# Performance work log

Measured on AMD Instinct MI355X. Metric: run time of the kernel, lower is better.

The kernel has to match this reference:

```python
import jax, jax.numpy as jnp
import numpy as np

B, D, C = 4096, 256, 32000
T = 1.0
P_MARGIN = 0.5
N_MARGIN = 0.5
W_BU = 1.0
W_MS = 0.0
SIM_CAP = 0.999999


def setup_inputs() -> dict:
    key = jax.random.key(0)
    k1, k2, k3, k4, k5 = jax.random.split(key, 5)
    inputs = jax.random.normal(k1, (B, D), dtype=jnp.float32)
    inputs = inputs / jnp.linalg.norm(inputs, axis=1, keepdims=True)  # re-id features are L2-normalized
    targets = jax.random.randint(k2, (B,), 0, C, dtype=jnp.int32)
    indexs = jnp.arange(B, dtype=jnp.int32)
    label_to_pairs = jax.random.randint(k3, (B, 2), 0, B, dtype=jnp.int32)
    all_label_to_clusterid = jax.random.randint(k4, (C,), 0, C, dtype=jnp.int32)
    V = jax.random.normal(k5, (C, D), dtype=jnp.float32)
    V = V / jnp.linalg.norm(V, axis=1, keepdims=True)  # memory bank rows kept unit-norm by EMA update
    return {"inputs": inputs, "targets": targets, "indexs": indexs,
            "label_to_pairs": label_to_pairs,
            "all_label_to_clusterid": all_label_to_clusterid, "V": V}


def _ms_loss(inputs, targets):
    # vectorized form of ExLoss.ms with ms_table=False:
    # psims[i] = sims[i, targets==targets[i]], nsims[i] = sims[i, targets!=targets[i]]
    sims = inputs @ inputs.T  # [B, B]
    pos = targets[:, None] == targets[None, :]
    neg = ~pos
    NEG_BIG = jnp.float32(-1e30)
    POS_BIG = jnp.float32(1e30)
    p_thrd = jnp.where(neg.any(axis=1),
                       jnp.where(neg, sims, NEG_BIG).max(axis=1),
                       jnp.float32(-3.0)) + P_MARGIN
    n_thrd = jnp.where(pos.any(axis=1),
                       jnp.where(pos, sims, POS_BIG).min(axis=1),
                       jnp.float32(3.0)) - N_MARGIN
    hp = pos & (sims < p_thrd[:, None])
    hn = neg & (sims > n_thrd[:, None]) & (sims < SIM_CAP)
    hp_cnt = hp.sum()
    hn_cnt = hn.sum()
    # BCE-with-logits: target 1 -> softplus(-x); target 0 -> softplus(x); mean over kept elems
    hp_loss = jnp.where(hp_cnt > 0,
                        jnp.where(hp, jax.nn.softplus(-sims), 0.0).sum()
                        / jnp.maximum(hp_cnt, 1).astype(sims.dtype),
                        jnp.float32(0.0))
    hn_loss = jnp.where(hn_cnt > 0,
                        jnp.where(hn, jax.nn.softplus(sims), 0.0).sum()
                        / jnp.maximum(hn_cnt, 1).astype(sims.dtype),
                        jnp.float32(0.0))
    return hp_loss + hn_loss


def reference(inputs, targets, indexs, label_to_pairs, all_label_to_clusterid, V):
    # Exclusive.forward: logits against the memory bank
    tsims = inputs @ V.T            # [B, C]
    outputs = tsims * T
    # bu cross-entropy (weight=None, mean reduction)
    logp = jax.nn.log_softmax(outputs, axis=-1)
    bu_loss = -jnp.take_along_axis(logp, targets[:, None].astype(jnp.int32), axis=1).mean()
    ms_loss = _ms_loss(inputs, targets)
    loss = W_MS * ms_loss + W_BU * bu_loss
    return (loss, outputs)
```

## Files before the change

### kernel.cpp

```cpp
#include <hip/hip_runtime.h>
#include <hip/hip_bf16.h>
#include <stdint.h>

#define NB 4096
#define ND 256
#define NC 32000

typedef __bf16 bf16x8 __attribute__((ext_vector_type(8)));
typedef float  f32x4  __attribute__((ext_vector_type(4)));

#define GLDS16(g, l)                                                          \
  __builtin_amdgcn_global_load_lds(                                           \
      (const __attribute__((address_space(1))) void*)(g),                     \
      (__attribute__((address_space(3))) void*)(l), 16, 0, 0)

__device__ __forceinline__ unsigned short f32_to_bf16(float f) {
  union { float f; uint32_t u; } v; v.f = f;
  uint32_t r = v.u + 0x7fffu + ((v.u >> 16) & 1u);
  return (unsigned short)(r >> 16);
}

__global__ void prep_kernel(const float* __restrict__ inA,
                            const float* __restrict__ inV,
                            unsigned short* __restrict__ outA,
                            unsigned short* __restrict__ outV,
                            float* __restrict__ rowsum,
                            float* __restrict__ loss) {
  int gid = blockIdx.x * blockDim.x + threadIdx.x;
  int stride = gridDim.x * blockDim.x;
  if (gid == 0) *loss = 0.f;
  for (int i = gid; i < NB; i += stride) rowsum[i] = 0.f;
  const int nA4 = NB * ND / 4;
  const int nV4 = NC * ND / 4;
  for (int i = gid; i < nA4 + nV4; i += stride) {
    float4 v = (i < nA4) ? ((const float4*)inA)[i]
                         : ((const float4*)inV)[i - nA4];
    ushort4 o;
    o.x = f32_to_bf16(v.x);
    o.y = f32_to_bf16(v.y);
    o.z = f32_to_bf16(v.z);
    o.w = f32_to_bf16(v.w);
    if (i < nA4) ((ushort4*)outA)[i] = o;
    else         ((ushort4*)outV)[i - nA4] = o;
  }
}

__global__ void __launch_bounds__(256)
gemm_expsum_kernel(const unsigned short* __restrict__ A,
                   const unsigned short* __restrict__ V,
                   float* __restrict__ out,
                   float* __restrict__ rowsum) {
  __shared__ unsigned short As[128 * 32];
  __shared__ unsigned short Bs[128 * 32];

  const int tid  = threadIdx.x;
  const int lane = tid & 63;
  const int wave = tid >> 6;
  const int wr   = wave >> 1;
  const int wc   = wave & 1;
  const int c16  = lane & 15;
  const int kq   = lane >> 4;

  const int brow = blockIdx.y * 128;
  const int bcol = blockIdx.x * 128;

  f32x4 acc[4][4];
#pragma unroll
  for (int m = 0; m < 4; ++m)
#pragma unroll
    for (int n = 0; n < 4; ++n)
      acc[m][n] = (f32x4){0.f, 0.f, 0.f, 0.f};

  const char* gA = (const char*)A + (size_t)(brow + (tid >> 2)) * (ND * 2) + (tid & 3) * 16;
  const char* gB = (const char*)V + (size_t)(bcol + (tid >> 2)) * (ND * 2) + (tid & 3) * 16;
  char* lA = (char*)As + wave * 1024;
  char* lB = (char*)Bs + wave * 1024;

  const char* aFragBase = (const char*)As + (wr * 64 + c16) * 64 + kq * 16;
  const char* bFragBase = (const char*)Bs + (wc * 64 + c16) * 64 + kq * 16;

  for (int kt = 0; kt < ND / 32; ++kt) {
    const int koff = kt * 64;
    GLDS16(gA + koff,            lA);
    GLDS16(gA + koff + 64 * 512, lA + 4096);
    GLDS16(gB + koff,            lB);
    GLDS16(gB + koff + 64 * 512, lB + 4096);
    __syncthreads();

    bf16x8 af[4], bfv[4];
#pragma unroll
    for (int m = 0; m < 4; ++m)
      af[m] = *(const bf16x8*)(aFragBase + m * 16 * 64);
#pragma unroll
    for (int n = 0; n < 4; ++n)
      bfv[n] = *(const bf16x8*)(bFragBase + n * 16 * 64);
#pragma unroll
    for (int m = 0; m < 4; ++m)
#pragma unroll
      for (int n = 0; n < 4; ++n)
        acc[m][n] = __builtin_amdgcn_mfma_f32_16x16x32_bf16(af[m], bfv[n],
                                                            acc[m][n], 0, 0, 0);
    __syncthreads();
  }

#pragma unroll
  for (int m = 0; m < 4; ++m) {
#pragma unroll
    for (int r = 0; r < 4; ++r) {
      const int grow = brow + wr * 64 + m * 16 + kq * 4 + r;
      float* po = out + (size_t)grow * NC + (bcol + wc * 64 + c16);
      float s = 0.f;
#pragma unroll
      for (int n = 0; n < 4; ++n) {
        float v = acc[m][n][r];
        po[n * 16] = v;
        s += __expf(v);
      }
      s += __shfl_xor(s, 1);
      s += __shfl_xor(s, 2);
      s += __shfl_xor(s, 4);
      s += __shfl_xor(s, 8);
      if (c16 == 0) atomicAdd(&rowsum[grow], s);
    }
  }
}

__global__ void finalize_kernel(const float* __restrict__ rowsum,
                                const float* __restrict__ out,
                                const int* __restrict__ targets,
                                float* __restrict__ loss) {
  int i = blockIdx.x * blockDim.x + threadIdx.x;
  float li = 0.f;
  if (i < NB) {
    float lse = logf(rowsum[i]);
    float xt  = out[(size_t)i * NC + targets[i]];
    li = lse - xt;
  }
#pragma unroll
  for (int o = 32; o > 0; o >>= 1) li += __shfl_down(li, o);
  __shared__ float wsum[4];
  int lane = threadIdx.x & 63, wv = threadIdx.x >> 6;
  if (lane == 0) wsum[wv] = li;
  __syncthreads();
  if (threadIdx.x == 0) {
    float s = wsum[0] + wsum[1] + wsum[2] + wsum[3];
    atomicAdd(loss, s * (1.0f / NB));
  }
}

extern "C" void kernel_launch(void* const* d_in, const int* in_sizes, int n_in,
                              void* d_out, int out_size, void* d_ws, size_t ws_size,
                              hipStream_t stream) {
  const float* inputs  = (const float*)d_in[0];
  const int*   targets = (const int*)d_in[1];
  const float* V       = (const float*)d_in[5];

  float* loss    = (float*)d_out;
  float* outputs = (float*)d_out + 1;

  char* ws = (char*)d_ws;
  unsigned short* Abf = (unsigned short*)ws;
  unsigned short* Vbf = (unsigned short*)(ws + (size_t)NB * ND * 2);
  float* rowsum = (float*)(ws + (size_t)NB * ND * 2 + (size_t)NC * ND * 2);

  hipLaunchKernelGGL(prep_kernel, dim3(2048), dim3(256), 0, stream,
                     inputs, V, Abf, Vbf, rowsum, loss);
  hipLaunchKernelGGL(gemm_expsum_kernel, dim3(NC / 128, NB / 128), dim3(256), 0, stream,
                     Abf, Vbf, outputs, rowsum);
  hipLaunchKernelGGL(finalize_kernel, dim3(NB / 256), dim3(256), 0, stream,
                     rowsum, outputs, targets, loss);
}
```

Baseline: 362.2 us.

## Load MFMA fragments directly from global, stage epilogue via LDS for float4 stores

Replaces the LDS-staged K loop with direct per-wave global loads of bf16 fragments into registers, double-buffered across K steps so there are no block-wide barriers. The epilogue transposes each 16x64 accumulator tile through a per-wave LDS buffer so every lane writes contiguous float4 rows of the output, instead of scattered scalar stores. The grid is also swapped so consecutive blocks walk rows of A while sharing a column tile of V. In exchange it gives up LDS data sharing between waves, so global and L2 read traffic goes up, and it uses more registers.

Measured after the change: 332.5 us. 1.09x faster.

```diff
diff --git a/kernel.cpp b/kernel.cpp
--- a/kernel.cpp
+++ b/kernel.cpp
@@ -8,11 +8,6 @@
 
 typedef __bf16 bf16x8 __attribute__((ext_vector_type(8)));
 typedef float  f32x4  __attribute__((ext_vector_type(4)));
-
-#define GLDS16(g, l)                                                          \
-  __builtin_amdgcn_global_load_lds(                                           \
-      (const __attribute__((address_space(1))) void*)(g),                     \
-      (__attribute__((address_space(3))) void*)(l), 16, 0, 0)
 
 __device__ __forceinline__ unsigned short f32_to_bf16(float f) {
   union { float f; uint32_t u; } v; v.f = f;
@@ -50,8 +45,7 @@
                    const unsigned short* __restrict__ V,
                    float* __restrict__ out,
                    float* __restrict__ rowsum) {
-  __shared__ unsigned short As[128 * 32];
-  __shared__ unsigned short Bs[128 * 32];
+  __shared__ float tls[4][16][68];
 
   const int tid  = threadIdx.x;
   const int lane = tid & 63;
@@ -61,8 +55,13 @@
   const int c16  = lane & 15;
   const int kq   = lane >> 4;
 
-  const int brow = blockIdx.y * 128;
-  const int bcol = blockIdx.x * 128;
+  const int brow = blockIdx.x * 128;
+  const int bcol = blockIdx.y * 128;
+
+  const __bf16* Ab = (const __bf16*)A;
+  const __bf16* Vb = (const __bf16*)V;
+  const __bf16* aBase = Ab + (size_t)(brow + wr * 64 + c16) * ND + kq * 8;
+  const __bf16* bBase = Vb + (size_t)(bcol + wc * 64 + c16) * ND + kq * 8;
 
   f32x4 acc[4][4];
 #pragma unroll
@@ -71,58 +70,64 @@
     for (int n = 0; n < 4; ++n)
       acc[m][n] = (f32x4){0.f, 0.f, 0.f, 0.f};
 
-  const char* gA = (const char*)A + (size_t)(brow + (tid >> 2)) * (ND * 2) + (tid & 3) * 16;
-  const char* gB = (const char*)V + (size_t)(bcol + (tid >> 2)) * (ND * 2) + (tid & 3) * 16;
-  char* lA = (char*)As + wave * 1024;
-  char* lB = (char*)Bs + wave * 1024;
+  bf16x8 a0[4], b0[4], a1[4], b1[4];
 
-  const char* aFragBase = (const char*)As + (wr * 64 + c16) * 64 + kq * 16;
-  const char* bFragBase = (const char*)Bs + (wc * 64 + c16) * 64 + kq * 16;
+#define LOADF(AF, BF, KT)                                                     \
+  do {                                                                        \
+    _Pragma("unroll")                                                         \
+    for (int m = 0; m < 4; ++m)                                               \
+      AF[m] = *(const bf16x8*)(aBase + (size_t)m * 16 * ND + (KT) * 32);      \
+    _Pragma("unroll")                                                         \
+    for (int n = 0; n < 4; ++n)                                               \
+      BF[n] = *(const bf16x8*)(bBase + (size_t)n * 16 * ND + (KT) * 32);      \
+  } while (0)
 
-  for (int kt = 0; kt < ND / 32; ++kt) {
-    const int koff = kt * 64;
-    GLDS16(gA + koff,            lA);
-    GLDS16(gA + koff + 64 * 512, lA + 4096);
-    GLDS16(gB + koff,            lB);
-    GLDS16(gB + koff + 64 * 512, lB + 4096);
-    __syncthreads();
+#define MFMAALL(AF, BF)                                                       \
+  do {                                                                        \
+    _Pragma("unroll")                                                         \
+    for (int m = 0; m < 4; ++m)                                               \
+      _Pragma("unroll")                                                       \
+      for (int n = 0; n < 4; ++n)                                             \
+        acc[m][n] = __builtin_amdgcn_mfma_f32_16x16x32_bf16(AF[m], BF[n],     \
+                                                            acc[m][n], 0, 0, 0); \
+  } while (0)
 
-    bf16x8 af[4], bfv[4];
+  LOADF(a0, b0, 0);
 #pragma unroll
-    for (int m = 0; m < 4; ++m)
-      af[m] = *(const bf16x8*)(aFragBase + m * 16 * 64);
-#pragma unroll
-    for (int n = 0; n < 4; ++n)
-      bfv[n] = *(const bf16x8*)(bFragBase + n * 16 * 64);
-#pragma unroll
-    for (int m = 0; m < 4; ++m)
-#pragma unroll
-      for (int n = 0; n < 4; ++n)
-        acc[m][n] = __builtin_amdgcn_mfma_f32_16x16x32_bf16(af[m], bfv[n],
-                                                            acc[m][n], 0, 0, 0);
-    __syncthreads();
+  for (int kt = 0; kt < 8; kt += 2) {
+    if (kt + 1 < 8) LOADF(a1, b1, kt + 1);
+    MFMAALL(a0, b0);
+    if (kt + 2 < 8) LOADF(a0, b0, kt + 2);
+    MFMAALL(a1, b1);
   }
 
 #pragma unroll
   for (int m = 0; m < 4; ++m) {
 #pragma unroll
-    for (int r = 0; r < 4; ++r) {
-      const int grow = brow + wr * 64 + m * 16 + kq * 4 + r;
-      float* po = out + (size_t)grow * NC + (bcol + wc * 64 + c16);
-      float s = 0.f;
+    for (int n = 0; n < 4; ++n)
 #pragma unroll
-      for (int n = 0; n < 4; ++n) {
-        float v = acc[m][n][r];
-        po[n * 16] = v;
-        s += __expf(v);
-      }
+      for (int r = 0; r < 4; ++r)
+        tls[wave][kq * 4 + r][n * 16 + c16] = acc[m][n][r];
+    asm volatile("s_waitcnt lgkmcnt(0)" ::: "memory");
+    __builtin_amdgcn_sched_barrier(0);
+#pragma unroll
+    for (int rr = 0; rr < 4; ++rr) {
+      const int lr = rr * 4 + kq;
+      float4 v = *(const float4*)&tls[wave][lr][c16 * 4];
+      const int grow = brow + wr * 64 + m * 16 + lr;
+      *(float4*)(out + (size_t)grow * NC + bcol + wc * 64 + c16 * 4) = v;
+      float s = __expf(v.x) + __expf(v.y) + __expf(v.z) + __expf(v.w);
       s += __shfl_xor(s, 1);
       s += __shfl_xor(s, 2);
       s += __shfl_xor(s, 4);
       s += __shfl_xor(s, 8);
       if (c16 == 0) atomicAdd(&rowsum[grow], s);
     }
+    asm volatile("s_waitcnt lgkmcnt(0)" ::: "memory");
+    __builtin_amdgcn_sched_barrier(0);
   }
+#undef LOADF
+#undef MFMAALL
 }
 
 __global__ void finalize_kernel(const float* __restrict__ rowsum,
@@ -165,7 +170,7 @@
 
   hipLaunchKernelGGL(prep_kernel, dim3(2048), dim3(256), 0, stream,
                      inputs, V, Abf, Vbf, rowsum, loss);
-  hipLaunchKernelGGL(gemm_expsum_kernel, dim3(NC / 128, NB / 128), dim3(256), 0, stream,
+  hipLaunchKernelGGL(gemm_expsum_kernel, dim3(NB / 128, NC / 128), dim3(256), 0, stream,
                      Abf, Vbf, outputs, rowsum);
   hipLaunchKernelGGL(finalize_kernel, dim3(NB / 256), dim3(256), 0, stream,
                      rowsum, outputs, targets, loss);
```
